# Performance work log

Measured on AMD Instinct MI355X. Metric: run time of the kernel, lower is better.

The kernel has to match this reference:

```python
import jax, jax.numpy as jnp
import numpy as np

B, N, D, DFC, EMB, L = 16, 1024, 128, 128, 64, 4
NHOPS = (1, 2, 3, 4)  # tatic='cont': nhop(i) = i + 1
EDGE_P = 0.03


def _make_adj(k):
    u = jax.random.uniform(k, (B, N, N))
    a = u < EDGE_P
    a = a | jnp.transpose(a, (0, 2, 1))          # undirected
    a = a | jnp.eye(N, dtype=bool)[None]         # self loops
    return a.astype(jnp.float32)


def setup_inputs() -> dict:
    key = jax.random.key(0)
    ks = jax.random.split(key, 16)
    s = 0.05
    x = jax.random.normal(ks[0], (B, N, 2 * EMB), jnp.float32)
    adj1 = _make_adj(ks[1])
    adj2 = _make_adj(ks[2])
    valid = jnp.ones((B, N), jnp.float32)
    embede_w = jax.random.normal(ks[3], (D, 2 * EMB)) * s
    gW = jax.random.normal(ks[4], (L, D, D)) * s
    gb = jnp.zeros((L, D), jnp.float32)
    gA = jax.random.normal(ks[5], (L, D, D)) * s
    gate_w = jax.random.normal(ks[6], (L, 1, 2 * D)) * s
    gate_b = jnp.zeros((L, 1), jnp.float32)
    fc0_w = jax.random.normal(ks[7], (DFC, D)) * s
    fc0_b = jnp.zeros((DFC,), jnp.float32)
    fc1_w = jax.random.normal(ks[8], (DFC, DFC)) * s
    fc1_b = jnp.zeros((DFC,), jnp.float32)
    fc2_w = jax.random.normal(ks[9], (DFC, DFC)) * s
    fc2_b = jnp.zeros((DFC,), jnp.float32)
    fc3_w = jax.random.normal(ks[10], (1, DFC)) * s
    fc3_b = jnp.zeros((1,), jnp.float32)
    return dict(x=x, adj1=adj1, adj2=adj2, valid=valid, embede_w=embede_w,
                gW=gW, gb=gb, gA=gA, gate_w=gate_w, gate_b=gate_b,
                fc0_w=fc0_w, fc0_b=fc0_b, fc1_w=fc1_w, fc1_b=fc1_b,
                fc2_w=fc2_w, fc2_b=fc2_b, fc3_w=fc3_w, fc3_b=fc3_b)


def _glema(x, adj, W, b, A, gw, gbias, nhop):
    h = x @ W.T + b                                        # [B,N,D]
    e = jnp.einsum('bjl,bkl->bjk', jnp.einsum('bjd,de->bje', h, A), h)
    e = e + jnp.transpose(e, (0, 2, 1))                    # undirected
    att = jnp.where(adj > 0, e, jnp.float32(0.0))
    att = jax.nn.softmax(att, axis=1) * adj                # softmax over dim 1, then adj mask
    az = jax.nn.relu(jnp.einsum('bij,bjd->bid', att, h))
    coeff = jax.nn.sigmoid(jnp.concatenate([h, az], -1) @ gw.T + gbias)  # [B,N,1]
    z = h
    for _ in range(nhop):
        az = jax.nn.relu(jnp.einsum('bij,bjd->bid', att, z))
        z = coeff * h + (1.0 - coeff) * az
    return z


def reference(x, adj1, adj2, valid, embede_w, gW, gb, gA, gate_w, gate_b,
              fc0_w, fc0_b, fc1_w, fc1_b, fc2_w, fc2_b, fc3_w, fc3_b):
    h = x @ embede_w.T                                     # embede (no bias)
    for k in range(L):                                     # branch='both': c_hs2 - c_hs1
        h1 = _glema(h, adj1, gW[k], gb[k], gA[k], gate_w[k], gate_b[k], NHOPS[k])
        h2 = _glema(h, adj2, gW[k], gb[k], gA[k], gate_w[k], gate_b[k], NHOPS[k])
        h = h2 - h1                                        # dropout p used in eval mode -> identity
    h = h * valid[..., None]
    pooled = h.sum(1) / valid.sum(1, keepdims=True)        # [B,D]
    y = jax.nn.relu(pooled @ fc0_w.T + fc0_b)
    y = jax.nn.relu(y @ fc1_w.T + fc1_b)
    y = jax.nn.relu(y @ fc2_w.T + fc2_b)
    y = jax.nn.sigmoid(y @ fc3_w.T + fc3_b)
    return y.reshape(-1)                                   # [B]
```

## Files before the change

kernel.cpp:

```cpp
#include <hip/hip_runtime.h>

typedef _Float16 half_t;
typedef _Float16 half8 __attribute__((ext_vector_type(8)));
typedef float floatx4 __attribute__((ext_vector_type(4)));

#define MFMA(a,b,c) __builtin_amdgcn_mfma_f32_16x16x32_f16(a,b,c,0,0,0)

#define NB 16
#define NLEN 1024
#define DD 128
#define BN (NB*NLEN)
#define BND ((size_t)NB*NLEN*DD)
#define EMP 1044

__global__ __launch_bounds__(256)
void k_cast(const float* __restrict__ gW, const float* __restrict__ gA,
            const float* __restrict__ Ew,
            half_t* __restrict__ Wf, half_t* __restrict__ STf, half_t* __restrict__ EwF) {
    int i = blockIdx.x * 256 + threadIdx.x;
    if (i < 65536) {
        Wf[i] = (half_t)gW[i];
        int base = i & ~16383;
        int lrem = i & 16383;
        int d = lrem >> 7, e = lrem & 127;
        STf[base + (e << 7) + d] = (half_t)(gA[i] + gA[base + (e << 7) + d]);
    } else {
        int j = i - 65536;
        EwF[j] = (half_t)Ew[j];
    }
}

__global__ __launch_bounds__(256)
void k_emb(const float* __restrict__ x, const half_t* __restrict__ EwF,
           half_t* __restrict__ h16) {
    __shared__ half_t htile[32 * 136];
    __shared__ half_t otile[32 * 136];
    int g = blockIdx.x * 32;
    int t = threadIdx.x;
    int w = t >> 6, l = t & 63, q = l >> 4, l15 = l & 15;
#pragma unroll
    for (int v = 0; v < 2; v++) {
        int idx = v * 256 + t; int r = idx >> 4, c8 = (idx & 15) * 8;
        const float* xp = &x[(size_t)(g + r) * DD + c8];
        float4 f0 = *(const float4*)xp;
        float4 f1 = *(const float4*)(xp + 4);
        half8 va;
        va[0] = (half_t)f0.x; va[1] = (half_t)f0.y; va[2] = (half_t)f0.z; va[3] = (half_t)f0.w;
        va[4] = (half_t)f1.x; va[5] = (half_t)f1.y; va[6] = (half_t)f1.z; va[7] = (half_t)f1.w;
        *(half8*)&htile[r * 136 + c8] = va;
    }
    __syncthreads();
    int rowh = (w & 1) * 16;
    int c0 = (w >> 1) * 4;
    half8 a1[4];
#pragma unroll
    for (int kc = 0; kc < 4; kc++) a1[kc] = *(const half8*)&htile[(rowh + l15) * 136 + kc * 32 + q * 8];
#pragma unroll
    for (int cc = 0; cc < 4; cc++) {
        int col = (c0 + cc) * 16 + l15;
        floatx4 a = {0.f, 0.f, 0.f, 0.f};
#pragma unroll
        for (int kc = 0; kc < 4; kc++) {
            half8 bf = *(const half8*)&EwF[((size_t)col << 7) + kc * 32 + q * 8];
            a = MFMA(a1[kc], bf, a);
        }
#pragma unroll
        for (int r = 0; r < 4; r++)
            otile[(rowh + q * 4 + r) * 136 + col] = (half_t)a[r];
    }
    __syncthreads();
#pragma unroll
    for (int v = 0; v < 2; v++) {
        int idx = v * 256 + t; int r = idx >> 4, c8 = (idx & 15) * 8;
        *(half8*)&h16[((size_t)(g + r) << 7) + c8] = *(const half8*)&otile[r * 136 + c8];
    }
}

__global__ __launch_bounds__(256)
void k_mask(const float* __restrict__ adj1, const float* __restrict__ adj2,
            unsigned short* __restrict__ mask16) {
    __shared__ float ls[4][1024];
    int tid = threadIdx.x;
    int bid = blockIdx.x;
    int w = tid >> 6, l = tid & 63;
    int R = bid * 4 + w;
    int br = R >> 14, nb = R & 16383;
    const float* arow = (br ? adj2 : adj1) + (size_t)nb * 1024;
#pragma unroll
    for (int c = 0; c < 4; c++)
        *(float4*)&ls[w][c * 256 + l * 4] = *(const float4*)&arow[c * 256 + l * 4];
    __syncthreads();
    unsigned m = 0u;
#pragma unroll
    for (int c = 0; c < 4; c++) {
        float4 v = *(const float4*)&ls[w][l * 16 + c * 4];
        m |= (v.x > 0.f ? 1u : 0u) << (c * 4);
        m |= (v.y > 0.f ? 1u : 0u) << (c * 4 + 1);
        m |= (v.z > 0.f ? 1u : 0u) << (c * 4 + 2);
        m |= (v.w > 0.f ? 1u : 0u) << (c * 4 + 3);
    }
    mask16[(size_t)R * 64 + l] = (unsigned short)m;
}

__global__ __launch_bounds__(256)
void k_proj(const half_t* __restrict__ pa, const half_t* __restrict__ pb,
            const half_t* __restrict__ Wf, const float* __restrict__ bias,
            const half_t* __restrict__ STf,
            half_t* __restrict__ hbr16, half_t* __restrict__ hbrT,
            half_t* __restrict__ hbrF, half_t* __restrict__ hSF) {
    __shared__ half_t htile[32 * 136];
    __shared__ half_t hbtile[32 * 136];
    int g = blockIdx.x * 32;
    int t = threadIdx.x;
    int w = t >> 6, l = t & 63, q = l >> 4, l15 = l & 15;
#pragma unroll
    for (int v = 0; v < 2; v++) {
        int idx = v * 256 + t; int r = idx >> 4, c8 = (idx & 15) * 8;
        half8 va = *(const half8*)&pa[((size_t)(g + r) << 7) + c8];
        if (pb) {
            half8 vb = *(const half8*)&pb[((size_t)(g + r) << 7) + c8];
            va = va - vb;
        }
        *(half8*)&htile[r * 136 + c8] = va;
    }
    __syncthreads();
    int rowh = (w & 1) * 16;
    int c0 = (w >> 1) * 4;
    half8 a1[4];
#pragma unroll
    for (int kc = 0; kc < 4; kc++) a1[kc] = *(const half8*)&htile[(rowh + l15) * 136 + kc * 32 + q * 8];
    floatx4 acc[4];
#pragma unroll
    for (int cc = 0; cc < 4; cc++) {
        int col = (c0 + cc) * 16 + l15;
        floatx4 a = {0.f, 0.f, 0.f, 0.f};
#pragma unroll
        for (int kc = 0; kc < 4; kc++) {
            half8 bf = *(const half8*)&Wf[((size_t)col << 7) + kc * 32 + q * 8];
            a = MFMA(a1[kc], bf, a);
        }
        float bv = bias[col];
        a.x += bv; a.y += bv; a.z += bv; a.w += bv;
        acc[cc] = a;
    }
#pragma unroll
    for (int cc = 0; cc < 4; cc++) {
        int col = (c0 + cc) * 16 + l15;
#pragma unroll
        for (int r = 0; r < 4; r++)
            hbtile[(rowh + q * 4 + r) * 136 + col] = (half_t)acc[cc][r];
    }
    __syncthreads();
    half8 a2[4];
#pragma unroll
    for (int kc = 0; kc < 4; kc++) a2[kc] = *(const half8*)&hbtile[(rowh + l15) * 136 + kc * 32 + q * 8];
#pragma unroll
    for (int cc = 0; cc < 4; cc++) {
        int col = (c0 + cc) * 16 + l15;
        floatx4 a = {0.f, 0.f, 0.f, 0.f};
#pragma unroll
        for (int kc = 0; kc < 4; kc++) {
            half8 bf = *(const half8*)&STf[((size_t)col << 7) + kc * 32 + q * 8];
            a = MFMA(a2[kc], bf, a);
        }
        acc[cc] = a;
    }
    __syncthreads();
#pragma unroll
    for (int cc = 0; cc < 4; cc++) {
        int col = (c0 + cc) * 16 + l15;
#pragma unroll
        for (int r = 0; r < 4; r++) htile[(rowh + q * 4 + r) * 136 + col] = (half_t)acc[cc][r];
    }
    __syncthreads();
#pragma unroll
    for (int v = 0; v < 2; v++) {
        int idx = v * 256 + t; int r = idx >> 4, c8 = (idx & 15) * 8;
        *(half8*)&hbr16[((size_t)(g + r) << 7) + c8] = *(const half8*)&hbtile[r * 136 + c8];
    }
    {
        int b_ = g >> 10, gi = g & 1023;
        int d = t >> 1, hh = t & 1;
        half8 r0, r1;
#pragma unroll
        for (int e = 0; e < 8; e++) {
            r0[e] = hbtile[(hh * 16 + e) * 136 + d];
            r1[e] = hbtile[(hh * 16 + 8 + e) * 136 + d];
        }
        half_t* op = hbrT + ((size_t)b_ * 128 + d) * 1024 + gi + hh * 16;
        *(half8*)op = r0;
        *(half8*)(op + 8) = r1;
    }
#pragma unroll
    for (int v = 0; v < 2; v++) {
        int fi = v * 256 + t;
        int g2 = fi >> 8, kc = (fi >> 6) & 3, li = fi & 63;
        int src = (g2 * 16 + (li & 15)) * 136 + kc * 32 + (li >> 4) * 8;
        size_t dst = (((size_t)(blockIdx.x * 2 + g2) * 4 + kc) << 10) + li * 8;
        *(half8*)&hbrF[dst] = *(const half8*)&hbtile[src];
        *(half8*)&hSF[dst]  = *(const half8*)&htile[src];
    }
}

__global__ __launch_bounds__(256)
void k_E(const half_t* __restrict__ hSF, const half_t* __restrict__ hbrF,
         const unsigned short* __restrict__ mask16, const half_t* __restrict__ hbrT,
         half_t* __restrict__ Dm, float* __restrict__ rsr, half_t* __restrict__ hbrsT) {
    int hw = blockIdx.y * 64 + blockIdx.x;
    int wk = (hw & 7) * 128 + (hw >> 3);
    int b = wk >> 6, s = wk & 63;
    int t = threadIdx.x, w = t >> 6, l = t & 63, q = l >> 4, l15 = l & 15;
    __shared__ half_t emS[16 * EMP];
    __shared__ float rsS[2][16];
    size_t Gb = (size_t)b * 64;
    half8 A[4];
#pragma unroll
    for (int kc = 0; kc < 4; kc++)
        A[kc] = *(const half8*)&hSF[(((Gb + s) * 4 + kc) << 10) + l * 8];
#pragma unroll 4
    for (int cg = 0; cg < 16; cg++) {
        int c0 = w * 256 + cg * 16;
        floatx4 a = {0.f, 0.f, 0.f, 0.f};
#pragma unroll
        for (int kc = 0; kc < 4; kc++) {
            half8 bf = *(const half8*)&hbrF[(((Gb + w * 16 + cg) * 4 + kc) << 10) + l * 8];
            a = MFMA(A[kc], bf, a);
        }
#pragma unroll
        for (int r = 0; r < 4; r++)
            emS[(q * 4 + r) * EMP + c0 + l15] = (half_t)a[r];
    }
    __syncthreads();
    const float CN = 0.000335462627903f;
#pragma unroll
    for (int tt = 0; tt < 8; tt++) {
        int task = tt * 4 + w;
        int rl = task >> 1, br = task & 1;
        size_t R = ((size_t)br << 14) + (size_t)b * 1024 + s * 16 + rl;
        unsigned mv = (unsigned)mask16[R * 64 + l];
        half8 e0 = *(const half8*)&emS[rl * EMP + l * 16];
        half8 e1 = *(const half8*)&emS[rl * EMP + l * 16 + 8];
        half8 o0, o1;
        float rs = 0.f;
#pragma unroll
        for (int c2 = 0; c2 < 8; c2++) {
            float v0 = ((mv >> c2) & 1u) ? __expf((float)e0[c2] - 8.f) : 0.f;
            float v1 = ((mv >> (c2 + 8)) & 1u) ? __expf((float)e1[c2] - 8.f) : 0.f;
            o0[c2] = (half_t)v0; o1[c2] = (half_t)v1;
            rs += v0 + v1;
        }
        *(half8*)&Dm[R * 1024 + l * 16] = o0;
        *(half8*)&Dm[R * 1024 + l * 16 + 8] = o1;
        int cn = __popc(mv);
        rs += __shfl_xor(rs, 1); rs += __shfl_xor(rs, 2);
        rs += __shfl_xor(rs, 4); rs += __shfl_xor(rs, 8);
        rs += __shfl_xor(rs, 16); rs += __shfl_xor(rs, 32);
        cn += __shfl_xor(cn, 1); cn += __shfl_xor(cn, 2);
        cn += __shfl_xor(cn, 4); cn += __shfl_xor(cn, 8);
        cn += __shfl_xor(cn, 16); cn += __shfl_xor(cn, 32);
        if (l == 0) {
            float rv = 1.f / (rs + (1024.f - (float)cn) * CN);
            rsr[R] = rv;
            rsS[br][rl] = rv;
        }
    }
    __syncthreads();
    {
        int d = t >> 1, br = t & 1;
        const half_t* hp = hbrT + ((size_t)b * 128 + d) * 1024 + s * 16;
        half8 a0 = *(const half8*)hp, a1 = *(const half8*)(hp + 8);
        half8 r0, r1;
#pragma unroll
        for (int e = 0; e < 8; e++) {
            r0[e] = (half_t)((float)a0[e] * rsS[br][e]);
            r1[e] = (half_t)((float)a1[e] * rsS[br][8 + e]);
        }
        half_t* op = hbrsT + (((size_t)((br << 4) + b)) * 128 + d) * 1024 + s * 16;
        *(half8*)op = r0;
        *(half8*)(op + 8) = r1;
    }
}

__global__ __launch_bounds__(512)
void k_azd(const half_t* __restrict__ Dm, const float* __restrict__ rsr,
           const half_t* __restrict__ BT, const half_t* __restrict__ hbr16,
           const float* __restrict__ gw, const float* __restrict__ gb_,
           float* __restrict__ cfb, half_t* __restrict__ outR, half_t* __restrict__ outT,
           int mode) {
    __shared__ union {
        struct { half_t A[2][64][72]; half_t B[2][128][72]; } s;
        half_t az[64][136];
    } sm;
    int t = threadIdx.x, w = t >> 6, l = t & 63, q = l >> 4, l15 = l & 15;
    int wi = w & 3, wd = w >> 2;
    int bid = blockIdx.x;
    int slice = bid & 31, tile = bid >> 5;
    int br = slice & 1, b = slice >> 1;
    int c = (br << 4) + b;
    int i0 = tile * 64;
    const half_t* Dp = Dm + ((size_t)c << 20) + (size_t)i0 * 1024;
    const half_t* Bp = BT + ((size_t)c << 17);
    int ar = t >> 3, ac = (t & 7) * 8;
    half8 ra0, rb0, rb1;
    ra0 = *(const half8*)&Dp[(size_t)ar * 1024 + ac];
    rb0 = *(const half8*)&Bp[(size_t)ar * 1024 + ac];
    rb1 = *(const half8*)&Bp[(size_t)(ar + 64) * 1024 + ac];
    *(half8*)&sm.s.A[0][ar][ac] = ra0;
    *(half8*)&sm.s.B[0][ar][ac] = rb0;
    *(half8*)&sm.s.B[0][ar + 64][ac] = rb1;
    __syncthreads();
    floatx4 acc[4] = {};
    for (int kt = 0; kt < 16; kt++) {
        int buf = kt & 1;
        if (kt < 15) {
            int ko = (kt + 1) * 64;
            ra0 = *(const half8*)&Dp[(size_t)ar * 1024 + ko + ac];
            rb0 = *(const half8*)&Bp[(size_t)ar * 1024 + ko + ac];
            rb1 = *(const half8*)&Bp[(size_t)(ar + 64) * 1024 + ko + ac];
        }
#pragma unroll
        for (int kk = 0; kk < 2; kk++) {
            half8 af = *(const half8*)&sm.s.A[buf][wi * 16 + l15][kk * 32 + q * 8];
#pragma unroll
            for (int nf = 0; nf < 4; nf++) {
                half8 bf = *(const half8*)&sm.s.B[buf][wd * 64 + nf * 16 + l15][kk * 32 + q * 8];
                acc[nf] = MFMA(af, bf, acc[nf]);
            }
        }
        __syncthreads();
        if (kt < 15) {
            int nbuf = buf ^ 1;
            *(half8*)&sm.s.A[nbuf][ar][ac] = ra0;
            *(half8*)&sm.s.B[nbuf][ar][ac] = rb0;
            *(half8*)&sm.s.B[nbuf][ar + 64][ac] = rb1;
            __syncthreads();
        }
    }
#pragma unroll
    for (int nf = 0; nf < 4; nf++)
#pragma unroll
        for (int r = 0; r < 4; r++)
            sm.az[wi * 16 + q * 4 + r][wd * 64 + nf * 16 + l15] = (half_t)acc[nf][r];
    __syncthreads();
#pragma unroll
    for (int it = 0; it < 2; it++) {
        int iloc = it * 32 + (t >> 4);
        int i = i0 + iloc;
        int nb = b * 1024 + i;
        int R = c * 1024 + i;
        half8 az8 = *(const half8*)&sm.az[iloc][l15 * 8];
        half8 hv8 = *(const half8*)&hbr16[((size_t)nb << 7) + l15 * 8];
        float av[8], hv[8];
#pragma unroll
        for (int d = 0; d < 8; d++) {
            av[d] = fmaxf((float)az8[d], 0.f);
            hv[d] = (float)hv8[d];
        }
        float cf;
        if (mode >= 3) {
            const float* g1 = gw + l15 * 8;
            const float* g2 = gw + 128 + l15 * 8;
            float dp = 0.f;
#pragma unroll
            for (int d = 0; d < 8; d++) dp += hv[d] * g1[d] + av[d] * g2[d];
            dp += __shfl_xor(dp, 1); dp += __shfl_xor(dp, 2);
            dp += __shfl_xor(dp, 4); dp += __shfl_xor(dp, 8);
            cf = 1.f / (1.f + __expf(-(dp + gb_[0])));
            if (l15 == 0) cfb[R] = cf;
        } else {
            cf = cfb[R];
        }
        if (mode == 2 || mode == 4) {
            half8 o;
#pragma unroll
            for (int d = 0; d < 8; d++) o[d] = (half_t)(cf * hv[d] + (1.f - cf) * av[d]);
            *(half8*)&outR[(size_t)R * DD + l15 * 8] = o;
        } else {
            float sc = rsr[R];
#pragma unroll
            for (int d = 0; d < 8; d++)
                sm.az[iloc][l15 * 8 + d] = (half_t)(sc * (cf * hv[d] + (1.f - cf) * av[d]));
        }
    }
    if (mode == 1 || mode == 3) {
        __syncthreads();
        int d = t & 127, g4 = t >> 7;
        half_t* op = outT + ((size_t)c * 128 + d) * 1024 + i0 + g4 * 16;
        half8 r0, r1;
#pragma unroll
        for (int e = 0; e < 8; e++) {
            r0[e] = sm.az[g4 * 16 + e][d];
            r1[e] = sm.az[g4 * 16 + 8 + e][d];
        }
        *(half8*)op = r0;
        *(half8*)(op + 8) = r1;
    }
}

__global__ __launch_bounds__(256)
void k_pool(const half_t* __restrict__ z2, const half_t* __restrict__ z1,
            const float* __restrict__ valid, float* __restrict__ part) {
    int b = blockIdx.y, s = blockIdx.x;
    int t = threadIdx.x, d = t & 127, hf = t >> 7;
    __shared__ float red[128];
    float acc = 0.f;
    int nbase = s * 128 + hf * 64;
    for (int n = nbase; n < nbase + 64; n++) {
        size_t gi = ((size_t)(b * 1024 + n) << 7) + d;
        acc += ((float)z2[gi] - (float)z1[gi]) * valid[b * 1024 + n];
    }
    if (hf) red[d] = acc;
    __syncthreads();
    if (!hf) part[(b * 8 + s) * 128 + d] = acc + red[d];
}

__global__ __launch_bounds__(128)
void k_mlp(const float* __restrict__ part, const float* __restrict__ valid,
           const float* __restrict__ w0, const float* __restrict__ b0,
           const float* __restrict__ w1, const float* __restrict__ b1,
           const float* __restrict__ w2, const float* __restrict__ b2,
           const float* __restrict__ w3, const float* __restrict__ b3,
           float* __restrict__ out) {
    int b = blockIdx.x, t = threadIdx.x;
    __shared__ float y0[DD], y1[DD];
    __shared__ float sred[2];
    float vs = 0.f;
    for (int n = t; n < NLEN; n += 128) vs += valid[b * NLEN + n];
    for (int off = 32; off; off >>= 1) vs += __shfl_down(vs, off);
    if ((t & 63) == 0) sred[t >> 6] = vs;
    __syncthreads();
    float vsum = sred[0] + sred[1];
    float acc = 0.f;
#pragma unroll
    for (int s = 0; s < 8; s++) acc += part[(b * 8 + s) * 128 + t];
    y0[t] = acc / vsum;
    __syncthreads();
    float a = b0[t];
    for (int k = 0; k < DD; k++) a += y0[k] * w0[t * DD + k];
    y1[t] = fmaxf(a, 0.f);
    __syncthreads();
    a = b1[t];
    for (int k = 0; k < DD; k++) a += y1[k] * w1[t * DD + k];
    y0[t] = fmaxf(a, 0.f);
    __syncthreads();
    a = b2[t];
    for (int k = 0; k < DD; k++) a += y0[k] * w2[t * DD + k];
    y1[t] = fmaxf(a, 0.f);
    __syncthreads();
    float pv = y1[t] * w3[t];
    for (int off = 32; off; off >>= 1) pv += __shfl_down(pv, off);
    if ((t & 63) == 0) sred[t >> 6] = pv;
    __syncthreads();
    if (t == 0) out[b] = 1.f / (1.f + __expf(-(sred[0] + sred[1] + b3[0])));
}

extern "C" void kernel_launch(void* const* d_in, const int* in_sizes, int n_in,
                              void* d_out, int out_size, void* d_ws, size_t ws_size,
                              hipStream_t stream) {
    (void)in_sizes; (void)n_in; (void)out_size; (void)ws_size;
    const float* x     = (const float*)d_in[0];
    const float* adj1  = (const float*)d_in[1];
    const float* adj2  = (const float*)d_in[2];
    const float* valid = (const float*)d_in[3];
    const float* Ew    = (const float*)d_in[4];
    const float* gW    = (const float*)d_in[5];
    const float* gb    = (const float*)d_in[6];
    const float* gA    = (const float*)d_in[7];
    const float* gatew = (const float*)d_in[8];
    const float* gateb = (const float*)d_in[9];
    const float* w0 = (const float*)d_in[10]; const float* b0 = (const float*)d_in[11];
    const float* w1 = (const float*)d_in[12]; const float* b1 = (const float*)d_in[13];
    const float* w2 = (const float*)d_in[14]; const float* b2 = (const float*)d_in[15];
    const float* w3 = (const float*)d_in[16]; const float* b3 = (const float*)d_in[17];
    float* out = (float*)d_out;

    char* p = (char*)d_ws;
    float* rsr  = (float*)p; p += 2 * BN * 4;
    float* cfb  = (float*)p; p += 2 * BN * 4;
    float* partb = (float*)p; p += (size_t)NB * 8 * 128 * 4;
    half_t* h16   = (half_t*)p; p += BND * 2;
    half_t* hbr16 = (half_t*)p; p += BND * 2;
    half_t* hbrF  = (half_t*)p; p += BND * 2;
    half_t* hSF   = (half_t*)p; p += BND * 2;
    half_t* hbrT  = (half_t*)p; p += BND * 2;
    half_t* hbrsT = (half_t*)p; p += 2 * BND * 2;
    half_t* zf    = (half_t*)p; p += 2 * BND * 2;
    half_t* zTA   = (half_t*)p; p += 2 * BND * 2;
    half_t* zTB   = (half_t*)p; p += 2 * BND * 2;
    unsigned short* mask16 = (unsigned short*)p; p += (size_t)2 * BN * 64 * 2;
    half_t* Dm   = (half_t*)p; p += (size_t)2 * BN * 1024 * 2;
    half_t* Wf16 = (half_t*)p; p += (size_t)4 * 128 * 128 * 2;
    half_t* ST16 = (half_t*)p; p += (size_t)4 * 128 * 128 * 2;
    half_t* EwF  = (half_t*)p; p += (size_t)128 * 128 * 2;

    k_cast<<<320, 256, 0, stream>>>(gW, gA, Ew, Wf16, ST16, EwF);
    k_emb<<<512, 256, 0, stream>>>(x, EwF, h16);
    k_mask<<<8192, 256, 0, stream>>>(adj1, adj2, mask16);

    for (int k = 0; k < 4; k++) {
        int nhop = k + 1;
        const half_t* pa = k ? (zf + BND) : h16;
        const half_t* pb = k ? zf : nullptr;
        k_proj<<<512, 256, 0, stream>>>(pa, pb, Wf16 + (size_t)k * 16384, gb + k * 128,
                                        ST16 + (size_t)k * 16384, hbr16, hbrT, hbrF, hSF);
        k_E<<<dim3(64, NB), 256, 0, stream>>>(hSF, hbrF, mask16, hbrT, Dm, rsr, hbrsT);
        if (nhop == 1) {
            k_azd<<<512, 512, 0, stream>>>(Dm, rsr, hbrsT, hbr16, gatew + k * 256, gateb + k,
                                           cfb, zf, (half_t*)nullptr, 4);
        } else {
            k_azd<<<512, 512, 0, stream>>>(Dm, rsr, hbrsT, hbr16, gatew + k * 256, gateb + k,
                                           cfb, (half_t*)nullptr, zTA, 3);
        }
        const half_t* srcT = zTA;
        for (int hop = 2; hop <= nhop; hop++) {
            if (hop == nhop) {
                k_azd<<<512, 512, 0, stream>>>(Dm, rsr, srcT, hbr16, gatew + k * 256, gateb + k,
                                               cfb, zf, (half_t*)nullptr, 2);
            } else {
                half_t* dT = (hop & 1) ? zTA : zTB;
                k_azd<<<512, 512, 0, stream>>>(Dm, rsr, srcT, hbr16, gatew + k * 256, gateb + k,
                                               cfb, (half_t*)nullptr, dT, 1);
                srcT = dT;
            }
        }
    }
    k_pool<<<dim3(8, NB), 256, 0, stream>>>(zf + BND, zf, valid, partb);
    k_mlp<<<16, 128, 0, stream>>>(partb, valid, w0, b0, w1, b1, w2, b2, w3, b3, out);
}
```

Before: 621.4 us.

## Store attention matrix and z operands in MFMA fragment layout, drop LDS staging in k_azd

k_E now writes the masked exp attention matrix and the scaled hbr operand directly in a pre-swizzled MFMA fragment layout, and reorganizes the softmax row-sum reduction across waves. k_azd loads A and B fragments straight from global memory with register double-buffering, dropping the LDS tiles and most __syncthreads. Intermediate z outputs are written in the same fragment layout. This removes LDS traffic and barriers in the hot hop GEMMs. In exchange, B fragments are no longer shared through LDS, so each wave fetches them redundantly from global or L2.

```diff
diff --git a/kernel.cpp b/kernel.cpp
--- a/kernel.cpp
+++ b/kernel.cpp
@@ -205,12 +205,14 @@
 __global__ __launch_bounds__(256)
 void k_E(const half_t* __restrict__ hSF, const half_t* __restrict__ hbrF,
          const unsigned short* __restrict__ mask16, const half_t* __restrict__ hbrT,
-         half_t* __restrict__ Dm, float* __restrict__ rsr, half_t* __restrict__ hbrsT) {
+         half_t* __restrict__ DmF, float* __restrict__ rsr, half_t* __restrict__ hbrsF) {
     int hw = blockIdx.y * 64 + blockIdx.x;
     int wk = (hw & 7) * 128 + (hw >> 3);
     int b = wk >> 6, s = wk & 63;
     int t = threadIdx.x, w = t >> 6, l = t & 63, q = l >> 4, l15 = l & 15;
     __shared__ half_t emS[16 * EMP];
+    __shared__ float rsP[4][16];
+    __shared__ int   cnP[4][16];
     __shared__ float rsS[2][16];
     size_t Gb = (size_t)b * 64;
     half8 A[4];
@@ -232,115 +234,102 @@
     }
     __syncthreads();
     const float CN = 0.000335462627903f;
-#pragma unroll
-    for (int tt = 0; tt < 8; tt++) {
-        int task = tt * 4 + w;
-        int rl = task >> 1, br = task & 1;
-        size_t R = ((size_t)br << 14) + (size_t)b * 1024 + s * 16 + rl;
-        unsigned mv = (unsigned)mask16[R * 64 + l];
-        half8 e0 = *(const half8*)&emS[rl * EMP + l * 16];
-        half8 e1 = *(const half8*)&emS[rl * EMP + l * 16 + 8];
-        half8 o0, o1;
-        float rs = 0.f;
-#pragma unroll
-        for (int c2 = 0; c2 < 8; c2++) {
-            float v0 = ((mv >> c2) & 1u) ? __expf((float)e0[c2] - 8.f) : 0.f;
-            float v1 = ((mv >> (c2 + 8)) & 1u) ? __expf((float)e1[c2] - 8.f) : 0.f;
-            o0[c2] = (half_t)v0; o1[c2] = (half_t)v1;
-            rs += v0 + v1;
-        }
-        *(half8*)&Dm[R * 1024 + l * 16] = o0;
-        *(half8*)&Dm[R * 1024 + l * 16 + 8] = o1;
-        int cn = __popc(mv);
-        rs += __shfl_xor(rs, 1); rs += __shfl_xor(rs, 2);
-        rs += __shfl_xor(rs, 4); rs += __shfl_xor(rs, 8);
-        rs += __shfl_xor(rs, 16); rs += __shfl_xor(rs, 32);
-        cn += __shfl_xor(cn, 1); cn += __shfl_xor(cn, 2);
-        cn += __shfl_xor(cn, 4); cn += __shfl_xor(cn, 8);
-        cn += __shfl_xor(cn, 16); cn += __shfl_xor(cn, 32);
-        if (l == 0) {
-            float rv = 1.f / (rs + (1024.f - (float)cn) * CN);
-            rsr[R] = rv;
-            rsS[br][rl] = rv;
-        }
-    }
-    __syncthreads();
     {
-        int d = t >> 1, br = t & 1;
+        int br = w & 1, jbase = (w >> 1) * 16;
+        size_t Rrow = ((size_t)br << 14) + (size_t)b * 1024 + s * 16 + l15;
+        size_t slotbase = (((size_t)(br * 16 + b) * 64 + s) << 5) << 9;
+        float rsl = 0.f;
+        int cnl = 0;
+        for (int jj = 0; jj < 16; jj++) {
+            int jt = jbase + jj;
+            half8 e = *(const half8*)&emS[l15 * EMP + jt * 32 + q * 8];
+            unsigned mw = (unsigned)mask16[Rrow * 64 + jt * 2 + (q >> 1)];
+            unsigned bits = (mw >> ((q & 1) * 8)) & 0xFFu;
+            half8 o;
+#pragma unroll
+            for (int d = 0; d < 8; d++) {
+                float v = ((bits >> d) & 1u) ? __expf((float)e[d] - 8.f) : 0.f;
+                o[d] = (half_t)v;
+                rsl += v;
+            }
+            cnl += __popc(bits);
+            *(half8*)&DmF[slotbase + (size_t)jt * 512 + l * 8] = o;
+        }
+        rsl += __shfl_xor(rsl, 16); rsl += __shfl_xor(rsl, 32);
+        cnl += __shfl_xor(cnl, 16); cnl += __shfl_xor(cnl, 32);
+        if (l < 16) { rsP[w][l] = rsl; cnP[w][l] = cnl; }
+    }
+    __syncthreads();
+    if (t < 32) {
+        int brx = t >> 4, row = t & 15;
+        float rs = rsP[brx][row] + rsP[brx + 2][row];
+        int cn = cnP[brx][row] + cnP[brx + 2][row];
+        float rv = 1.f / (rs + (1024.f - (float)cn) * CN);
+        rsr[((size_t)brx << 14) + (size_t)b * 1024 + s * 16 + row] = rv;
+        rsS[brx][row] = rv;
+    }
+    __syncthreads();
+    {
+        int d = t >> 1, brx = t & 1;
+        int nf = d >> 4, dd = d & 15, qo = (s & 1) * 2;
         const half_t* hp = hbrT + ((size_t)b * 128 + d) * 1024 + s * 16;
         half8 a0 = *(const half8*)hp, a1 = *(const half8*)(hp + 8);
         half8 r0, r1;
 #pragma unroll
         for (int e = 0; e < 8; e++) {
-            r0[e] = (half_t)((float)a0[e] * rsS[br][e]);
-            r1[e] = (half_t)((float)a1[e] * rsS[br][8 + e]);
-        }
-        half_t* op = hbrsT + (((size_t)((br << 4) + b)) * 128 + d) * 1024 + s * 16;
-        *(half8*)op = r0;
-        *(half8*)(op + 8) = r1;
+            r0[e] = (half_t)((float)a0[e] * rsS[brx][e]);
+            r1[e] = (half_t)((float)a1[e] * rsS[brx][8 + e]);
+        }
+        size_t slot = (((size_t)((brx << 4) + b) * 256 + (s >> 1) * 8 + nf)) << 9;
+        *(half8*)&hbrsF[slot + (qo * 16 + dd) * 8] = r0;
+        *(half8*)&hbrsF[slot + ((qo + 1) * 16 + dd) * 8] = r1;
     }
 }
 
 __global__ __launch_bounds__(512)
-void k_azd(const half_t* __restrict__ Dm, const float* __restrict__ rsr,
-           const half_t* __restrict__ BT, const half_t* __restrict__ hbr16,
+void k_azd(const half_t* __restrict__ DmF, const float* __restrict__ rsr,
+           const half_t* __restrict__ zF, const half_t* __restrict__ hbr16,
            const float* __restrict__ gw, const float* __restrict__ gb_,
-           float* __restrict__ cfb, half_t* __restrict__ outR, half_t* __restrict__ outT,
+           float* __restrict__ cfb, half_t* __restrict__ outR, half_t* __restrict__ outF,
            int mode) {
-    __shared__ union {
-        struct { half_t A[2][64][72]; half_t B[2][128][72]; } s;
-        half_t az[64][136];
-    } sm;
+    __shared__ half_t az[64][136];
     int t = threadIdx.x, w = t >> 6, l = t & 63, q = l >> 4, l15 = l & 15;
-    int wi = w & 3, wd = w >> 2;
+    int wi = w & 3, dh = w >> 2;
     int bid = blockIdx.x;
     int slice = bid & 31, tile = bid >> 5;
     int br = slice & 1, b = slice >> 1;
     int c = (br << 4) + b;
     int i0 = tile * 64;
-    const half_t* Dp = Dm + ((size_t)c << 20) + (size_t)i0 * 1024;
-    const half_t* Bp = BT + ((size_t)c << 17);
-    int ar = t >> 3, ac = (t & 7) * 8;
-    half8 ra0, rb0, rb1;
-    ra0 = *(const half8*)&Dp[(size_t)ar * 1024 + ac];
-    rb0 = *(const half8*)&Bp[(size_t)ar * 1024 + ac];
-    rb1 = *(const half8*)&Bp[(size_t)(ar + 64) * 1024 + ac];
-    *(half8*)&sm.s.A[0][ar][ac] = ra0;
-    *(half8*)&sm.s.B[0][ar][ac] = rb0;
-    *(half8*)&sm.s.B[0][ar + 64][ac] = rb1;
-    __syncthreads();
+    const half_t* Ap = DmF + (size_t)(c * 64 + tile * 4 + wi) * 16384 + l * 8;
+    const half_t* Bp = zF + ((size_t)c * 256 + dh * 4) * 512 + l * 8;
     floatx4 acc[4] = {};
-    for (int kt = 0; kt < 16; kt++) {
-        int buf = kt & 1;
-        if (kt < 15) {
-            int ko = (kt + 1) * 64;
-            ra0 = *(const half8*)&Dp[(size_t)ar * 1024 + ko + ac];
-            rb0 = *(const half8*)&Bp[(size_t)ar * 1024 + ko + ac];
-            rb1 = *(const half8*)&Bp[(size_t)(ar + 64) * 1024 + ko + ac];
-        }
-#pragma unroll
-        for (int kk = 0; kk < 2; kk++) {
-            half8 af = *(const half8*)&sm.s.A[buf][wi * 16 + l15][kk * 32 + q * 8];
-#pragma unroll
-            for (int nf = 0; nf < 4; nf++) {
-                half8 bf = *(const half8*)&sm.s.B[buf][wd * 64 + nf * 16 + l15][kk * 32 + q * 8];
-                acc[nf] = MFMA(af, bf, acc[nf]);
-            }
-        }
-        __syncthreads();
-        if (kt < 15) {
-            int nbuf = buf ^ 1;
-            *(half8*)&sm.s.A[nbuf][ar][ac] = ra0;
-            *(half8*)&sm.s.B[nbuf][ar][ac] = rb0;
-            *(half8*)&sm.s.B[nbuf][ar + 64][ac] = rb1;
-            __syncthreads();
-        }
+    half8 aC = *(const half8*)Ap;
+    half8 bC0 = *(const half8*)(Bp);
+    half8 bC1 = *(const half8*)(Bp + 512);
+    half8 bC2 = *(const half8*)(Bp + 1024);
+    half8 bC3 = *(const half8*)(Bp + 1536);
+    for (int jt = 0; jt < 32; jt++) {
+        half8 aN = aC, bN0 = bC0, bN1 = bC1, bN2 = bC2, bN3 = bC3;
+        if (jt < 31) {
+            const half_t* An = Ap + (size_t)(jt + 1) * 512;
+            const half_t* Bn = Bp + (size_t)(jt + 1) * 4096;
+            aN  = *(const half8*)An;
+            bN0 = *(const half8*)(Bn);
+            bN1 = *(const half8*)(Bn + 512);
+            bN2 = *(const half8*)(Bn + 1024);
+            bN3 = *(const half8*)(Bn + 1536);
+        }
+        acc[0] = MFMA(aC, bC0, acc[0]);
+        acc[1] = MFMA(aC, bC1, acc[1]);
+        acc[2] = MFMA(aC, bC2, acc[2]);
+        acc[3] = MFMA(aC, bC3, acc[3]);
+        aC = aN; bC0 = bN0; bC1 = bN1; bC2 = bN2; bC3 = bN3;
     }
 #pragma unroll
     for (int nf = 0; nf < 4; nf++)
 #pragma unroll
         for (int r = 0; r < 4; r++)
-            sm.az[wi * 16 + q * 4 + r][wd * 64 + nf * 16 + l15] = (half_t)acc[nf][r];
+            az[wi * 16 + q * 4 + r][dh * 64 + nf * 16 + l15] = (half_t)acc[nf][r];
     __syncthreads();
 #pragma unroll
     for (int it = 0; it < 2; it++) {
@@ -348,7 +337,7 @@
         int i = i0 + iloc;
         int nb = b * 1024 + i;
         int R = c * 1024 + i;
-        half8 az8 = *(const half8*)&sm.az[iloc][l15 * 8];
+        half8 az8 = *(const half8*)&az[iloc][l15 * 8];
         half8 hv8 = *(const half8*)&hbr16[((size_t)nb << 7) + l15 * 8];
         float av[8], hv[8];
 #pragma unroll
@@ -379,21 +368,22 @@
             float sc = rsr[R];
 #pragma unroll
             for (int d = 0; d < 8; d++)
-                sm.az[iloc][l15 * 8 + d] = (half_t)(sc * (cf * hv[d] + (1.f - cf) * av[d]));
+                az[iloc][l15 * 8 + d] = (half_t)(sc * (cf * hv[d] + (1.f - cf) * av[d]));
         }
     }
     if (mode == 1 || mode == 3) {
         __syncthreads();
         int d = t & 127, g4 = t >> 7;
-        half_t* op = outT + ((size_t)c * 128 + d) * 1024 + i0 + g4 * 16;
+        int q0 = (g4 & 1) * 2;
+        size_t slot = ((size_t)c * 256 + ((i0 >> 5) + (g4 >> 1)) * 8 + (d >> 4)) << 9;
         half8 r0, r1;
 #pragma unroll
         for (int e = 0; e < 8; e++) {
-            r0[e] = sm.az[g4 * 16 + e][d];
-            r1[e] = sm.az[g4 * 16 + 8 + e][d];
-        }
-        *(half8*)op = r0;
-        *(half8*)(op + 8) = r1;
+            r0[e] = az[g4 * 16 + e][d];
+            r1[e] = az[g4 * 16 + 8 + e][d];
+        }
+        *(half8*)&outF[slot + (q0 * 16 + (d & 15)) * 8] = r0;
+        *(half8*)&outF[slot + ((q0 + 1) * 16 + (d & 15)) * 8] = r1;
     }
 }
 
@@ -483,12 +473,12 @@
     half_t* hbrF  = (half_t*)p; p += BND * 2;
     half_t* hSF   = (half_t*)p; p += BND * 2;
     half_t* hbrT  = (half_t*)p; p += BND * 2;
-    half_t* hbrsT = (half_t*)p; p += 2 * BND * 2;
+    half_t* hbrsF = (half_t*)p; p += 2 * BND * 2;
     half_t* zf    = (half_t*)p; p += 2 * BND * 2;
-    half_t* zTA   = (half_t*)p; p += 2 * BND * 2;
-    half_t* zTB   = (half_t*)p; p += 2 * BND * 2;
+    half_t* zFA   = (half_t*)p; p += 2 * BND * 2;
+    half_t* zFB   = (half_t*)p; p += 2 * BND * 2;
     unsigned short* mask16 = (unsigned short*)p; p += (size_t)2 * BN * 64 * 2;
-    half_t* Dm   = (half_t*)p; p += (size_t)2 * BN * 1024 * 2;
+    half_t* DmF  = (half_t*)p; p += (size_t)2 * BN * 1024 * 2;
     half_t* Wf16 = (half_t*)p; p += (size_t)4 * 128 * 128 * 2;
     half_t* ST16 = (half_t*)p; p += (size_t)4 * 128 * 128 * 2;
     half_t* EwF  = (half_t*)p; p += (size_t)128 * 128 * 2;
@@ -503,24 +493,24 @@
         const half_t* pb = k ? zf : nullptr;
         k_proj<<<512, 256, 0, stream>>>(pa, pb, Wf16 + (size_t)k * 16384, gb + k * 128,
                                         ST16 + (size_t)k * 16384, hbr16, hbrT, hbrF, hSF);
-        k_E<<<dim3(64, NB), 256, 0, stream>>>(hSF, hbrF, mask16, hbrT, Dm, rsr, hbrsT);
+        k_E<<<dim3(64, NB), 256, 0, stream>>>(hSF, hbrF, mask16, hbrT, DmF, rsr, hbrsF);
         if (nhop == 1) {
-            k_azd<<<512, 512, 0, stream>>>(Dm, rsr, hbrsT, hbr16, gatew + k * 256, gateb + k,
+            k_azd<<<512, 512, 0, stream>>>(DmF, rsr, hbrsF, hbr16, gatew + k * 256, gateb + k,
                                            cfb, zf, (half_t*)nullptr, 4);
         } else {
-            k_azd<<<512, 512, 0, stream>>>(Dm, rsr, hbrsT, hbr16, gatew + k * 256, gateb + k,
-                                           cfb, (half_t*)nullptr, zTA, 3);
-        }
-        const half_t* srcT = zTA;
+            k_azd<<<512, 512, 0, stream>>>(DmF, rsr, hbrsF, hbr16, gatew + k * 256, gateb + k,
+                                           cfb, (half_t*)nullptr, zFA, 3);
+        }
+        const half_t* srcF = zFA;
         for (int hop = 2; hop <= nhop; hop++) {
             if (hop == nhop) {
-                k_azd<<<512, 512, 0, stream>>>(Dm, rsr, srcT, hbr16, gatew + k * 256, gateb + k,
+                k_azd<<<512, 512, 0, stream>>>(DmF, rsr, srcF, hbr16, gatew + k * 256, gateb + k,
                                                cfb, zf, (half_t*)nullptr, 2);
             } else {
-                half_t* dT = (hop & 1) ? zTA : zTB;
-                k_azd<<<512, 512, 0, stream>>>(Dm, rsr, srcT, hbr16, gatew + k * 256, gateb + k,
-                                               cfb, (half_t*)nullptr, dT, 1);
-                srcT = dT;
+                half_t* dF = (hop & 1) ? zFA : zFB;
+                k_azd<<<512, 512, 0, stream>>>(DmF, rsr, srcF, hbr16, gatew + k * 256, gateb + k,
+                                               cfb, (half_t*)nullptr, dF, 1);
+                srcF = dF;
             }
         }
     }
```

New measurement: 634.8 us. 1.02x slower.
